# Kernel optimization log

Measured on AMD Instinct MI355X. Metric: run time of the kernel, lower is better.

The kernel has to match this reference:

```python
import jax, jax.numpy as jnp
import numpy as np

BS = 131072
NX = 4       # num_dim_x (p, theta, v, omega)
NU = 1       # num_dim_control
H = 256      # n_hidden


def segway_dynamics(x):
    # x: [bs, 4] -> f: [bs, 4], g: [bs, 4, 1]
    theta, v, omega = x[:, 1], x[:, 2], x[:, 3]
    c, s = jnp.cos(theta), jnp.sin(theta)
    f2 = (c * (9.8 * s + 11.5 * v) + 68.4 * v - 1.2 * omega ** 2 * s) / (c - 24.7)
    f3 = (-58.8 * v * c - 243.5 * v - s * (208.3 + omega ** 2 * c)) / (c ** 2 - 24.7)
    f = jnp.stack([v, omega, f2, f3], axis=1)
    g2 = (-1.8 * c - 10.9) / (c - 24.7)
    g3 = (9.3 * c + 38.6) / (c ** 2 - 24.7)
    zero = jnp.zeros_like(g2)
    g = jnp.stack([zero, zero, g2, g3], axis=1)[:, :, None]
    return f, g


def setup_inputs() -> dict:
    key = jax.random.key(0)
    ks = jax.random.split(key, 13)
    d = {"x": jax.random.normal(ks[0], (BS, NX), dtype=jnp.float32)}
    shapes = {
        "Vw1": (H, NX), "Vb1": (H,),
        "Vw2": (H, H),  "Vb2": (H,),
        "Vw3": (H // 4, H), "Vb3": (H // 4,),
        "Uw1": (H, NX), "Ub1": (H,),
        "Uw2": (H, H),  "Ub2": (H,),
        "Uw3": (NU, H), "Ub3": (NU,),
    }
    for i, (name, shp) in enumerate(shapes.items()):
        d[name] = jax.random.normal(ks[i + 1], shp, dtype=jnp.float32) * 0.05
    return d


def reference(x, Vw1, Vb1, Vw2, Vb2, Vw3, Vb3, Uw1, Ub1, Uw2, Ub2, Uw3, Ub3):
    # --- Lyapunov value + analytic gradient ---
    a1 = jnp.tanh(x @ Vw1.T + Vb1)          # [bs, H]
    a2 = jnp.tanh(a1 @ Vw2.T + Vb2)         # [bs, H]
    a3 = jnp.tanh(a2 @ Vw3.T + Vb3)         # [bs, H//4]
    V = 0.5 * jnp.sum(a3 * a3, axis=1)      # [bs]
    # diag_embed(1-tanh^2) @ W  ==  (1-tanh^2)[:, :, None] * W  (no dense diag)
    D1 = (1.0 - a1 ** 2)[:, :, None] * Vw1[None]                          # [bs, H, 4]
    D2 = (1.0 - a2 ** 2)[:, :, None] * jnp.einsum('ij,bjk->bik', Vw2, D1)  # [bs, H, 4]
    D3 = (1.0 - a3 ** 2)[:, :, None] * jnp.einsum('ij,bjk->bik', Vw3, D2)  # [bs, H/4, 4]
    grad_V = jnp.einsum('bi,bij->bj', a3, D3)  # [bs, 4]

    # --- learned controls ---
    u1 = jnp.tanh(x @ Uw1.T + Ub1)
    u2 = jnp.tanh(u1 @ Uw2.T + Ub2)
    u = jnp.tanh(u2 @ Uw3.T + Ub3) * 20.0     # [bs, 1]

    # --- Lie derivatives / Vdot ---
    f, g = segway_dynamics(x)
    L_f_V = jnp.sum(grad_V * f, axis=1, keepdims=True)    # [bs, 1]
    L_g_V = jnp.einsum('bi,bic->bc', grad_V, g)           # [bs, 1]
    Vdot = (L_f_V + jnp.sum(L_g_V * u, axis=1, keepdims=True))[:, :, None]  # [bs,1,1]
    return u, V, Vdot
```

## Files before the change

kernel.cpp:

```cpp
#include <hip/hip_runtime.h>
#include <hip/hip_bf16.h>

#define BSZ 131072

typedef __bf16 v8bf __attribute__((ext_vector_type(8)));
typedef float f32x4 __attribute__((ext_vector_type(4)));

constexpr int RPB = 64;
constexpr int NTHREADS = 512;
constexpr int LDA = 264;

constexpr int OFF_B2T = 0;
constexpr int OFF_U2T = 65536;
constexpr int OFF_B2  = 131072;
constexpr int OFF_B3T = 196608;
constexpr int OFF_B3  = 212992;
constexpr int OFF_U3  = 229376;
constexpr int OFF_GV  = 233472;
constexpr int OFF_LV1 = 237568;
constexpr int OFF_LU1 = 245760;
constexpr int WS_ELEMS = 253952;

__device__ __forceinline__ float tanhf_fast(float x){
  float e = __expf(2.0f * x);
  return 1.0f - 2.0f * __builtin_amdgcn_rcpf(e + 1.0f);
}

__device__ __forceinline__ __bf16 f2bf(float f){
  unsigned u = __builtin_bit_cast(unsigned, f);
  u += 0x8000u;
  unsigned short h = (unsigned short)(u >> 16);
  return __builtin_bit_cast(__bf16, h);
}

__device__ __forceinline__ unsigned pk2bf(float lo, float hi){
  unsigned r;
  asm("v_cvt_pk_bf16_f32 %0, %1, %2" : "=v"(r) : "v"(lo), "v"(hi));
  return r;
}
__device__ __forceinline__ float bflo(unsigned u){ return __builtin_bit_cast(float, u << 16); }
__device__ __forceinline__ float bfhi(unsigned u){ return __builtin_bit_cast(float, u & 0xffff0000u); }

__global__ void prep_weights(const float* __restrict__ Vw2,
                             const float* __restrict__ Uw2,
                             const float* __restrict__ Vw3,
                             const float* __restrict__ Vw1,
                             const float* __restrict__ Uw1,
                             const float* __restrict__ Uw3,
                             __bf16* __restrict__ ws){
  int e = blockIdx.x * 256 + threadIdx.x;
  if (e >= WS_ELEMS) return;
  int idx, NT, base, mode; const float* W;
  if      (e <  65536){ idx = e;          W = Vw2; mode = 0; NT = 16; base = OFF_B2T; }
  else if (e < 131072){ idx = e - 65536;  W = Uw2; mode = 0; NT = 16; base = OFF_U2T; }
  else if (e < 196608){ idx = e - 131072; W = Vw2; mode = 1; NT = 16; base = OFF_B2;  }
  else if (e < 212992){ idx = e - 196608; W = Vw3; mode = 0; NT = 4;  base = OFF_B3T; }
  else if (e < 229376){ idx = e - 212992; W = Vw3; mode = 1; NT = 16; base = OFF_B3;  }
  else if (e < 233472){ idx = e - 229376; W = Uw3; mode = 2; NT = 1;  base = OFF_U3;  }
  else if (e < 237568){ idx = e - 233472; W = Vw1; mode = 3; NT = 1;  base = OFF_GV;  }
  else if (e < 245760){ idx = e - 237568; W = Vw1; mode = 4; NT = 16; base = OFF_LV1; }
  else                { idx = e - 245760; W = Uw1; mode = 4; NT = 16; base = OFF_LU1; }
  int j = idx & 7, l = (idx >> 3) & 63, f = idx >> 9;
  int nt = f % NT, ks = f / NT;
  int k = ks * 32 + (l >> 4) * 8 + j;
  int n = nt * 16 + (l & 15);
  float v;
  if      (mode == 0) v = W[n * 256 + k];
  else if (mode == 1) v = W[k * 256 + n];
  else if (mode == 2) v = (n == 0) ? W[k] : 0.0f;
  else if (mode == 3) v = (n < 4)  ? W[k * 4 + n] : 0.0f;
  else                v = (k < 4)  ? W[n * 4 + k] : 0.0f;
  ws[base + idx] = f2bf(v);
}

__global__ __launch_bounds__(NTHREADS, 4) void fused_clf(
    const float* __restrict__ x,
    const float* __restrict__ Vb1, const float* __restrict__ Vb2,
    const float* __restrict__ Vb3,
    const float* __restrict__ Ub1, const float* __restrict__ Ub2,
    const float* __restrict__ Ub3,
    const __bf16* __restrict__ ws,
    float* __restrict__ out)
{
  __shared__ alignas(16) __bf16 b1[RPB][LDA];
  __shared__ alignas(16) __bf16 b2[RPB][LDA];
  __shared__ union alignas(16) S3 {
    __bf16 b3[RPB][72];
    float  r4[8][RPB][4];
  } s3;
  __shared__ alignas(16) float red[RPB][4];
  __shared__ float utile[RPB];

  const int tid  = threadIdx.x;
  const int lane = tid & 63;
  const int wave = tid >> 6;
  const int quad = lane >> 4;
  const int l16  = lane & 15;
  const int row0 = blockIdx.x * RPB;

  v8bf xa[4];
  #pragma unroll
  for (int m = 0; m < 4; m++){
    v8bf z;
    #pragma unroll
    for (int j = 0; j < 8; j++) z[j] = (__bf16)0.0f;
    if (quad == 0){
      float4 xv = ((const float4*)x)[row0 + m*16 + l16];
      z[0] = f2bf(xv.x); z[1] = f2bf(xv.y); z[2] = f2bf(xv.z); z[3] = f2bf(xv.w);
    }
    xa[m] = z;
  }


  auto layer1m = [&](const __bf16* __restrict__ Bw, const float* __restrict__ bv,
                     __bf16 (*dst)[LDA]){
    const v8bf* B = (const v8bf*)Bw;
    v8bf bf0 = B[(wave*2 + 0)*64 + lane];
    v8bf bf1 = B[(wave*2 + 1)*64 + lane];
    f32x4 acc[4][2];
    #pragma unroll
    for (int m = 0; m < 4; m++){ f32x4 z={0.f,0.f,0.f,0.f}; acc[m][0]=z; acc[m][1]=z; }
    #pragma unroll
    for (int m = 0; m < 4; m++){
      acc[m][0] = __builtin_amdgcn_mfma_f32_16x16x32_bf16(bf0, xa[m], acc[m][0], 0,0,0);
      acc[m][1] = __builtin_amdgcn_mfma_f32_16x16x32_bf16(bf1, xa[m], acc[m][1], 0,0,0);
    }
    #pragma unroll
    for (int nt = 0; nt < 2; nt++){
      const int f0 = (wave*2 + nt)*16 + quad*4;
      f32x4 bvv = ((const f32x4*)bv)[f0 >> 2];
      #pragma unroll
      for (int m = 0; m < 4; m++){
        const int brow = m*16 + l16;
        uint2 pk;
        pk.x = pk2bf(tanhf_fast(acc[m][nt][0] + bvv[0]),
                     tanhf_fast(acc[m][nt][1] + bvv[1]));
        pk.y = pk2bf(tanhf_fast(acc[m][nt][2] + bvv[2]),
                     tanhf_fast(acc[m][nt][3] + bvv[3]));
        *(uint2*)&dst[brow][f0] = pk;
      }
    }
  };

  auto gemm256 = [&](const __bf16 (*A)[LDA], const __bf16* __restrict__ Bw,
                     const float* __restrict__ bias, __bf16 (*dst)[LDA], int epi){
    f32x4 acc[4][2];
    #pragma unroll
    for (int m = 0; m < 4; m++){ f32x4 z={0.f,0.f,0.f,0.f}; acc[m][0]=z; acc[m][1]=z; }
    const v8bf* B = (const v8bf*)Bw;
    #pragma unroll
    for (int kk = 0; kk < 8; kk++){
      v8bf a[4];
      #pragma unroll
      for (int m = 0; m < 4; m++)
        a[m] = *(const v8bf*)&A[m*16 + l16][kk*32 + quad*8];
      #pragma unroll
      for (int nt = 0; nt < 2; nt++){
        v8bf bf = B[(kk*16 + wave*2 + nt)*64 + lane];
        #pragma unroll
        for (int m = 0; m < 4; m++)
          acc[m][nt] = __builtin_amdgcn_mfma_f32_16x16x32_bf16(bf, a[m], acc[m][nt], 0,0,0);
      }
    }
    #pragma unroll
    for (int nt = 0; nt < 2; nt++){
      const int f0 = (wave*2 + nt)*16 + quad*4;
      f32x4 bvv = {0.f,0.f,0.f,0.f};
      if (epi == 0) bvv = ((const f32x4*)bias)[f0 >> 2];
      #pragma unroll
      for (int m = 0; m < 4; m++){
        const int brow = m*16 + l16;
        uint2 pk;
        if (epi == 0){
          pk.x = pk2bf(tanhf_fast(acc[m][nt][0] + bvv[0]),
                       tanhf_fast(acc[m][nt][1] + bvv[1]));
          pk.y = pk2bf(tanhf_fast(acc[m][nt][2] + bvv[2]),
                       tanhf_fast(acc[m][nt][3] + bvv[3]));
        } else {
          uint2 old = *(const uint2*)&dst[brow][f0];
          float a0 = bflo(old.x), a1 = bfhi(old.x);
          float c0 = bflo(old.y), c1 = bfhi(old.y);
          pk.x = pk2bf(acc[m][nt][0] * (1.0f - a0*a0),
                       acc[m][nt][1] * (1.0f - a1*a1));
          pk.y = pk2bf(acc[m][nt][2] * (1.0f - c0*c0),
                       acc[m][nt][3] * (1.0f - c1*c1));
        }
        *(uint2*)&dst[brow][f0] = pk;
      }
    }
  };

  auto mfma_reduce = [&](const __bf16 (*A)[LDA], const __bf16* __restrict__ Bw,
                         int ncols){
    f32x4 acc[4];
    #pragma unroll
    for (int m = 0; m < 4; m++){ f32x4 z={0.f,0.f,0.f,0.f}; acc[m]=z; }
    const v8bf* B = (const v8bf*)Bw;
    v8bf bf = B[wave*64 + lane];
    #pragma unroll
    for (int m = 0; m < 4; m++){
      v8bf a = *(const v8bf*)&A[m*16 + l16][wave*32 + quad*8];
      acc[m] = __builtin_amdgcn_mfma_f32_16x16x32_bf16(bf, a, acc[m], 0,0,0);
    }
    if (quad == 0){
      if (ncols == 4){
        #pragma unroll
        for (int m = 0; m < 4; m++)
          *(f32x4*)&s3.r4[wave][m*16 + l16][0] = acc[m];
      } else {
        #pragma unroll
        for (int m = 0; m < 4; m++)
          s3.r4[wave][m*16 + l16][0] = acc[m][0];
      }
    }
  };

  layer1m(ws + OFF_LU1, Ub1, b2);
  __syncthreads();
  gemm256(b2, ws + OFF_U2T, Ub2, b1, 0);
  __syncthreads();
  mfma_reduce(b1, ws + OFF_U3, 1);
  __syncthreads();
  if (tid < RPB){
    float z = Ub3[0];
    #pragma unroll
    for (int w = 0; w < 8; w++) z += s3.r4[w][tid][0];
    float u = tanhf_fast(z) * 20.0f;
    utile[tid] = u;
    out[row0 + tid] = u;
  }
  layer1m(ws + OFF_LV1, Vb1, b1);
  __syncthreads();
  gemm256(b1, ws + OFF_B2T, Vb2, b2, 0);
  __syncthreads();

  {
    const int mp = wave >> 2;
    const int nt = wave & 3;
    f32x4 acc[2];
    { f32x4 z={0.f,0.f,0.f,0.f}; acc[0]=z; acc[1]=z; }
    const v8bf* B = (const v8bf*)(ws + OFF_B3T);
    #pragma unroll
    for (int kk = 0; kk < 8; kk++){
      v8bf bf = B[(kk*4 + nt)*64 + lane];
      #pragma unroll
      for (int m2 = 0; m2 < 2; m2++){
        v8bf a = *(const v8bf*)&b2[(mp*2 + m2)*16 + l16][kk*32 + quad*8];
        acc[m2] = __builtin_amdgcn_mfma_f32_16x16x32_bf16(bf, a, acc[m2], 0,0,0);
      }
    }
    const int f0 = nt*16 + quad*4;
    f32x4 bvv = ((const f32x4*)Vb3)[f0 >> 2];
    #pragma unroll
    for (int m2 = 0; m2 < 2; m2++){
      const int brow = (mp*2 + m2)*16 + l16;
      float t0 = tanhf_fast(acc[m2][0] + bvv[0]);
      float t1 = tanhf_fast(acc[m2][1] + bvv[1]);
      float t2 = tanhf_fast(acc[m2][2] + bvv[2]);
      float t3 = tanhf_fast(acc[m2][3] + bvv[3]);
      float s0 = t0*t0, s1 = t1*t1, s2 = t2*t2, s3q = t3*t3;
      float sq = (s0 + s1) + (s2 + s3q);
      sq += __shfl_xor(sq, 16);
      sq += __shfl_xor(sq, 32);
      if (quad == 0) red[brow][nt] = sq;
      uint2 pk;
      pk.x = pk2bf(t0*(1.0f - s0), t1*(1.0f - s1));
      pk.y = pk2bf(t2*(1.0f - s2), t3*(1.0f - s3q));
      *(uint2*)&s3.b3[brow][f0] = pk;
    }
  }
  __syncthreads();

  {
    f32x4 acc[4][2];
    #pragma unroll
    for (int m = 0; m < 4; m++){ f32x4 z={0.f,0.f,0.f,0.f}; acc[m][0]=z; acc[m][1]=z; }
    const v8bf* B = (const v8bf*)(ws + OFF_B3);
    #pragma unroll
    for (int kk = 0; kk < 2; kk++){
      v8bf a[4];
      #pragma unroll
      for (int m = 0; m < 4; m++)
        a[m] = *(const v8bf*)&s3.b3[m*16 + l16][kk*32 + quad*8];
      #pragma unroll
      for (int nt = 0; nt < 2; nt++){
        v8bf bf = B[(kk*16 + wave*2 + nt)*64 + lane];
        #pragma unroll
        for (int m = 0; m < 4; m++)
          acc[m][nt] = __builtin_amdgcn_mfma_f32_16x16x32_bf16(bf, a[m], acc[m][nt], 0,0,0);
      }
    }
    #pragma unroll
    for (int nt = 0; nt < 2; nt++){
      const int f0 = (wave*2 + nt)*16 + quad*4;
      #pragma unroll
      for (int m = 0; m < 4; m++){
        const int brow = m*16 + l16;
        uint2 old = *(const uint2*)&b2[brow][f0];
        float a0 = bflo(old.x), a1 = bfhi(old.x);
        float c0 = bflo(old.y), c1 = bfhi(old.y);
        uint2 pk;
        pk.x = pk2bf(acc[m][nt][0] * (1.0f - a0*a0),
                     acc[m][nt][1] * (1.0f - a1*a1));
        pk.y = pk2bf(acc[m][nt][2] * (1.0f - c0*c0),
                     acc[m][nt][3] * (1.0f - c1*c1));
        *(uint2*)&b2[brow][f0] = pk;
      }
    }
    if (tid < RPB)
      out[BSZ + row0 + tid] = 0.5f * (red[tid][0] + red[tid][1] + red[tid][2] + red[tid][3]);
  }
  __syncthreads();

  gemm256(b2, ws + OFF_B2, nullptr, b1, 1);
  __syncthreads();
  mfma_reduce(b1, ws + OFF_GV, 4);
  __syncthreads();
  if (tid < 256){
    int b = tid >> 2, k2 = tid & 3;
    float s = 0.f;
    #pragma unroll
    for (int w = 0; w < 8; w++) s += s3.r4[w][b][k2];
    red[b][k2] = s;
  }
  __syncthreads();

  if (tid < RPB){
    float4 xv = ((const float4*)x)[row0 + tid];
    float th = xv.y, vv = xv.z, om = xv.w;
    float c, s;
    __sincosf(th, &s, &c);
    float rdc  = __builtin_amdgcn_rcpf(c - 24.7f);
    float rdc2 = __builtin_amdgcn_rcpf(c*c - 24.7f);
    float f2v = (c*(9.8f*s + 11.5f*vv) + 68.4f*vv - 1.2f*om*om*s) * rdc;
    float f3v = (-58.8f*vv*c - 243.5f*vv - s*(208.3f + om*om*c)) * rdc2;
    float g2v = (-1.8f*c - 10.9f) * rdc;
    float g3v = (9.3f*c + 38.6f) * rdc2;
    f32x4 rv = *(const f32x4*)&red[tid][0];
    float Lf = rv[0]*vv + rv[1]*om + rv[2]*f2v + rv[3]*f3v;
    float Lg = rv[2]*g2v + rv[3]*g3v;
    out[2*BSZ + row0 + tid] = Lf + Lg * utile[tid];
  }
}

extern "C" void kernel_launch(void* const* d_in, const int* in_sizes, int n_in,
                              void* d_out, int out_size, void* d_ws, size_t ws_size,
                              hipStream_t stream) {
  const float* x   = (const float*)d_in[0];
  const float* Vw1 = (const float*)d_in[1];
  const float* Vb1 = (const float*)d_in[2];
  const float* Vw2 = (const float*)d_in[3];
  const float* Vb2 = (const float*)d_in[4];
  const float* Vw3 = (const float*)d_in[5];
  const float* Vb3 = (const float*)d_in[6];
  const float* Uw1 = (const float*)d_in[7];
  const float* Ub1 = (const float*)d_in[8];
  const float* Uw2 = (const float*)d_in[9];
  const float* Ub2 = (const float*)d_in[10];
  const float* Uw3 = (const float*)d_in[11];
  const float* Ub3 = (const float*)d_in[12];
  __bf16* ws = (__bf16*)d_ws;
  float* out = (float*)d_out;

  hipLaunchKernelGGL(prep_weights, dim3((WS_ELEMS + 255) / 256), dim3(256), 0, stream,
                     Vw2, Uw2, Vw3, Vw1, Uw1, Uw3, ws);
  hipLaunchKernelGGL(fused_clf, dim3(BSZ / RPB), dim3(NTHREADS), 0, stream,
                     x, Vb1, Vb2, Vb3, Ub1, Ub2, Ub3, ws, out);
}
```

Before: 166.3 us.

## Fuse control output layer into U2 GEMM epilogue, reorder stages, add MFMA priority

The U-network's final 256->1 projection is folded into the epilogue of the second-layer GEMM as an FP32 dot product with shuffle reduction. This removes a layer-2 activation writeback, a separate MFMA reduce pass, and one barrier. The two first-layer computations are now issued back to back, and the u-finalisation overlaps the V second-layer GEMM, cutting barriers further. Also adds s_setprio around MFMA loops and an exp2-based tanh with fma, which may shift register pressure and wave scheduling.

Result: faster. 161.2 us, median of 2 (-3.0%).

```diff
diff --git a/kernel.cpp b/kernel.cpp
--- a/kernel.cpp
+++ b/kernel.cpp
@@ -22,8 +22,8 @@
 constexpr int WS_ELEMS = 253952;
 
 __device__ __forceinline__ float tanhf_fast(float x){
-  float e = __expf(2.0f * x);
-  return 1.0f - 2.0f * __builtin_amdgcn_rcpf(e + 1.0f);
+  float e = __builtin_amdgcn_exp2f(x * 2.885390082f);
+  return __builtin_fmaf(-2.0f, __builtin_amdgcn_rcpf(e + 1.0f), 1.0f);
 }
 
 __device__ __forceinline__ __bf16 f2bf(float f){
@@ -78,7 +78,7 @@
     const float* __restrict__ Vb1, const float* __restrict__ Vb2,
     const float* __restrict__ Vb3,
     const float* __restrict__ Ub1, const float* __restrict__ Ub2,
-    const float* __restrict__ Ub3,
+    const float* __restrict__ Ub3, const float* __restrict__ Uw3,
     const __bf16* __restrict__ ws,
     float* __restrict__ out)
 {
@@ -120,11 +120,13 @@
     f32x4 acc[4][2];
     #pragma unroll
     for (int m = 0; m < 4; m++){ f32x4 z={0.f,0.f,0.f,0.f}; acc[m][0]=z; acc[m][1]=z; }
+    __builtin_amdgcn_s_setprio(1);
     #pragma unroll
     for (int m = 0; m < 4; m++){
       acc[m][0] = __builtin_amdgcn_mfma_f32_16x16x32_bf16(bf0, xa[m], acc[m][0], 0,0,0);
       acc[m][1] = __builtin_amdgcn_mfma_f32_16x16x32_bf16(bf1, xa[m], acc[m][1], 0,0,0);
     }
+    __builtin_amdgcn_s_setprio(0);
     #pragma unroll
     for (int nt = 0; nt < 2; nt++){
       const int f0 = (wave*2 + nt)*16 + quad*4;
@@ -148,6 +150,7 @@
     #pragma unroll
     for (int m = 0; m < 4; m++){ f32x4 z={0.f,0.f,0.f,0.f}; acc[m][0]=z; acc[m][1]=z; }
     const v8bf* B = (const v8bf*)Bw;
+    __builtin_amdgcn_s_setprio(1);
     #pragma unroll
     for (int kk = 0; kk < 8; kk++){
       v8bf a[4];
@@ -162,6 +165,7 @@
           acc[m][nt] = __builtin_amdgcn_mfma_f32_16x16x32_bf16(bf, a[m], acc[m][nt], 0,0,0);
       }
     }
+    __builtin_amdgcn_s_setprio(0);
     #pragma unroll
     for (int nt = 0; nt < 2; nt++){
       const int f0 = (wave*2 + nt)*16 + quad*4;
@@ -190,37 +194,78 @@
     }
   };
 
-  auto mfma_reduce = [&](const __bf16 (*A)[LDA], const __bf16* __restrict__ Bw,
-                         int ncols){
+  auto u2dot = [&](const __bf16 (*A)[LDA], const __bf16* __restrict__ Bw,
+                   const float* __restrict__ bias, const float* __restrict__ w3){
+    f32x4 acc[4][2];
+    #pragma unroll
+    for (int m = 0; m < 4; m++){ f32x4 z={0.f,0.f,0.f,0.f}; acc[m][0]=z; acc[m][1]=z; }
+    const v8bf* B = (const v8bf*)Bw;
+    __builtin_amdgcn_s_setprio(1);
+    #pragma unroll
+    for (int kk = 0; kk < 8; kk++){
+      v8bf a[4];
+      #pragma unroll
+      for (int m = 0; m < 4; m++)
+        a[m] = *(const v8bf*)&A[m*16 + l16][kk*32 + quad*8];
+      #pragma unroll
+      for (int nt = 0; nt < 2; nt++){
+        v8bf bf = B[(kk*16 + wave*2 + nt)*64 + lane];
+        #pragma unroll
+        for (int m = 0; m < 4; m++)
+          acc[m][nt] = __builtin_amdgcn_mfma_f32_16x16x32_bf16(bf, a[m], acc[m][nt], 0,0,0);
+      }
+    }
+    __builtin_amdgcn_s_setprio(0);
+    float part[4] = {0.f, 0.f, 0.f, 0.f};
+    #pragma unroll
+    for (int nt = 0; nt < 2; nt++){
+      const int f0 = (wave*2 + nt)*16 + quad*4;
+      f32x4 bvv = ((const f32x4*)bias)[f0 >> 2];
+      f32x4 w3v = ((const f32x4*)w3)[f0 >> 2];
+      #pragma unroll
+      for (int m = 0; m < 4; m++)
+        #pragma unroll
+        for (int r = 0; r < 4; r++)
+          part[m] = __builtin_fmaf(tanhf_fast(acc[m][nt][r] + bvv[r]), w3v[r], part[m]);
+    }
+    #pragma unroll
+    for (int m = 0; m < 4; m++){
+      part[m] += __shfl_xor(part[m], 16);
+      part[m] += __shfl_xor(part[m], 32);
+    }
+    if (quad == 0){
+      #pragma unroll
+      for (int m = 0; m < 4; m++)
+        s3.r4[wave][m*16 + l16][0] = part[m];
+    }
+  };
+
+  auto mfma_reduce4 = [&](const __bf16 (*A)[LDA], const __bf16* __restrict__ Bw){
     f32x4 acc[4];
     #pragma unroll
     for (int m = 0; m < 4; m++){ f32x4 z={0.f,0.f,0.f,0.f}; acc[m]=z; }
     const v8bf* B = (const v8bf*)Bw;
     v8bf bf = B[wave*64 + lane];
+    __builtin_amdgcn_s_setprio(1);
     #pragma unroll
     for (int m = 0; m < 4; m++){
       v8bf a = *(const v8bf*)&A[m*16 + l16][wave*32 + quad*8];
       acc[m] = __builtin_amdgcn_mfma_f32_16x16x32_bf16(bf, a, acc[m], 0,0,0);
     }
+    __builtin_amdgcn_s_setprio(0);
     if (quad == 0){
-      if (ncols == 4){
-        #pragma unroll
-        for (int m = 0; m < 4; m++)
-          *(f32x4*)&s3.r4[wave][m*16 + l16][0] = acc[m];
-      } else {
-        #pragma unroll
-        for (int m = 0; m < 4; m++)
-          s3.r4[wave][m*16 + l16][0] = acc[m][0];
-      }
+      #pragma unroll
+      for (int m = 0; m < 4; m++)
+        *(f32x4*)&s3.r4[wave][m*16 + l16][0] = acc[m];
     }
   };
 
   layer1m(ws + OFF_LU1, Ub1, b2);
-  __syncthreads();
-  gemm256(b2, ws + OFF_U2T, Ub2, b1, 0);
-  __syncthreads();
-  mfma_reduce(b1, ws + OFF_U3, 1);
-  __syncthreads();
+  layer1m(ws + OFF_LV1, Vb1, b1);
+  __syncthreads();
+  u2dot(b2, ws + OFF_U2T, Ub2, Uw3);
+  __syncthreads();
+  gemm256(b1, ws + OFF_B2T, Vb2, b2, 0);
   if (tid < RPB){
     float z = Ub3[0];
     #pragma unroll
@@ -229,9 +274,6 @@
     utile[tid] = u;
     out[row0 + tid] = u;
   }
-  layer1m(ws + OFF_LV1, Vb1, b1);
-  __syncthreads();
-  gemm256(b1, ws + OFF_B2T, Vb2, b2, 0);
   __syncthreads();
 
   {
@@ -240,6 +282,7 @@
     f32x4 acc[2];
     { f32x4 z={0.f,0.f,0.f,0.f}; acc[0]=z; acc[1]=z; }
     const v8bf* B = (const v8bf*)(ws + OFF_B3T);
+    __builtin_amdgcn_s_setprio(1);
     #pragma unroll
     for (int kk = 0; kk < 8; kk++){
       v8bf bf = B[(kk*4 + nt)*64 + lane];
@@ -249,6 +292,7 @@
         acc[m2] = __builtin_amdgcn_mfma_f32_16x16x32_bf16(bf, a, acc[m2], 0,0,0);
       }
     }
+    __builtin_amdgcn_s_setprio(0);
     const int f0 = nt*16 + quad*4;
     f32x4 bvv = ((const f32x4*)Vb3)[f0 >> 2];
     #pragma unroll
@@ -276,6 +320,7 @@
     #pragma unroll
     for (int m = 0; m < 4; m++){ f32x4 z={0.f,0.f,0.f,0.f}; acc[m][0]=z; acc[m][1]=z; }
     const v8bf* B = (const v8bf*)(ws + OFF_B3);
+    __builtin_amdgcn_s_setprio(1);
     #pragma unroll
     for (int kk = 0; kk < 2; kk++){
       v8bf a[4];
@@ -290,6 +335,7 @@
           acc[m][nt] = __builtin_amdgcn_mfma_f32_16x16x32_bf16(bf, a[m], acc[m][nt], 0,0,0);
       }
     }
+    __builtin_amdgcn_s_setprio(0);
     #pragma unroll
     for (int nt = 0; nt < 2; nt++){
       const int f0 = (wave*2 + nt)*16 + quad*4;
@@ -314,7 +360,7 @@
 
   gemm256(b2, ws + OFF_B2, nullptr, b1, 1);
   __syncthreads();
-  mfma_reduce(b1, ws + OFF_GV, 4);
+  mfma_reduce4(b1, ws + OFF_GV);
   __syncthreads();
   if (tid < 256){
     int b = tid >> 2, k2 = tid & 3;
@@ -365,5 +411,5 @@
   hipLaunchKernelGGL(prep_weights, dim3((WS_ELEMS + 255) / 256), dim3(256), 0, stream,
                      Vw2, Uw2, Vw3, Vw1, Uw1, Uw3, ws);
   hipLaunchKernelGGL(fused_clf, dim3(BSZ / RPB), dim3(NTHREADS), 0, stream,
-                     x, Vb1, Vb2, Vb3, Ub1, Ub2, Ub3, ws, out);
-}
+                     x, Vb1, Vb2, Vb3, Ub1, Ub2, Ub3, Uw3, ws, out);
+}
```
